# Optimization experiments

Measured on AMD Instinct MI355X. Metric: run time of the kernel, lower is better.

The kernel has to match this reference:

```python
import jax, jax.numpy as jnp
import numpy as np

N = 100000
E = 1600000
IN_DIM = 256
OUT_DIM = 128
LEAKY_SLOPE = 0.01  # torch nn.LeakyReLU default


def setup_inputs() -> dict:
    key = jax.random.key(0)
    k1, k2, k3, k4, k5 = jax.random.split(key, 5)
    features = jax.random.normal(k1, (N, IN_DIM), dtype=jnp.float32)
    # xavier_uniform for weight [out, in]
    limit = float(np.sqrt(6.0 / (IN_DIM + OUT_DIM)))
    weight = jax.random.uniform(k2, (OUT_DIM, IN_DIM), dtype=jnp.float32,
                                minval=-limit, maxval=limit)
    edge_rows = jnp.sort(jax.random.randint(k3, (E,), 0, N, dtype=jnp.int32))
    edge_cols = jax.random.randint(k4, (E,), 0, N, dtype=jnp.int32)
    edge_vals = jax.random.uniform(k5, (E,), dtype=jnp.float32)
    return {"features": features, "weight": weight,
            "edge_rows": edge_rows, "edge_cols": edge_cols,
            "edge_vals": edge_vals}


def reference(features, weight, edge_rows, edge_cols, edge_vals):
    # support = LeakyReLU(features @ W^T)   [N, OUT_DIM]
    support = jax.nn.leaky_relu(jnp.einsum('ni,oi->no', features, weight),
                                negative_slope=LEAKY_SLOPE)
    # SpMM: out[r] = sum over edges (r, c, v) of v * support[c]
    msgs = support[edge_cols] * edge_vals[:, None]  # [E, OUT_DIM]
    out = jax.ops.segment_sum(msgs, edge_rows, num_segments=N)
    return out
```

## Files before the change

### kernel.cpp

```cpp
#include <hip/hip_runtime.h>

#define IN_DIM 256
#define OUT_DIM 128
#define LEAKY 0.01f
#define GEMM_BLOCKS 512

typedef __attribute__((ext_vector_type(8))) short bf16x8;
typedef __attribute__((ext_vector_type(4))) float f32x4;
typedef __attribute__((ext_vector_type(4))) unsigned u32x4;

__device__ inline unsigned cvtpk_bf16(float lo, float hi) {
  unsigned r;
  asm volatile("v_cvt_pk_bf16_f32 %0, %1, %2" : "=v"(r) : "v"(lo), "v"(hi));
  return r;
}

__device__ inline float blo(unsigned u) {
  union { unsigned x; float f; } c; c.x = u << 16; return c.f;
}
__device__ inline float bhi(unsigned u) {
  union { unsigned x; float f; } c; c.x = u & 0xFFFF0000u; return c.f;
}
__device__ inline float asf(unsigned u) {
  union { unsigned x; float f; } c; c.x = u; return c.f;
}

__device__ inline int swz_byte(int r, int u) {
  return r * 512 + ((u & 16) << 4) + (((u & 15) ^ (r & 15)) << 4);
}

__global__ __launch_bounds__(512, 4) void gemm_scan_pack(
    const float* __restrict__ feat, const float* __restrict__ w,
    const int* __restrict__ erows, const int* __restrict__ ecols,
    const float* __restrict__ evals, unsigned short* __restrict__ support,
    int* __restrict__ rs, unsigned* __restrict__ ev, int nrows, int nedges,
    int ntiles, int scan_blocks) {
  if (blockIdx.x >= GEMM_BLOCKS) {
    const int sb = blockIdx.x - GEMM_BLOCKS;
    if (sb < scan_blocks) {
      const int i = sb * 512 + threadIdx.x;
      if (i >= nedges) return;
      const int cur  = erows[i];
      const int prev = (i == 0) ? -1 : erows[i - 1];
      for (int r = prev + 1; r <= cur; ++r) rs[r] = i;
      if (i == nedges - 1)
        for (int r = cur + 1; r <= nrows; ++r) rs[r] = nedges;
    } else {
      const int p = (sb - scan_blocks) * 512 + threadIdx.x;
      if (p * 2 + 1 >= nedges) {
        if (p * 2 < nedges) {
          ev[p * 4 + 0] = (unsigned)ecols[p * 2];
          ev[p * 4 + 1] = __float_as_uint(evals[p * 2]);
        }
        return;
      }
      const int2   c2 = *reinterpret_cast<const int2*>(&ecols[p * 2]);
      const float2 v2 = *reinterpret_cast<const float2*>(&evals[p * 2]);
      uint4 o;
      o.x = (unsigned)c2.x;
      o.y = __float_as_uint(v2.x);
      o.z = (unsigned)c2.y;
      o.w = __float_as_uint(v2.y);
      reinterpret_cast<uint4*>(ev)[p] = o;
    }
    return;
  }

  __shared__ alignas(16) unsigned short wlds[128 * 256];
  char* wb = reinterpret_cast<char*>(wlds);

  const int t = threadIdx.x;
#pragma unroll
  for (int it = 0; it < 8; ++it) {
    const int g = it * 512 + t;
    const int r = g >> 5;
    const int u = g & 31;
    const float* src = w + r * IN_DIM + u * 8;
    const float4 a = *reinterpret_cast<const float4*>(src);
    const float4 b = *reinterpret_cast<const float4*>(src + 4);
    uint4 pk;
    pk.x = cvtpk_bf16(a.x, a.y);
    pk.y = cvtpk_bf16(a.z, a.w);
    pk.z = cvtpk_bf16(b.x, b.y);
    pk.w = cvtpk_bf16(b.z, b.w);
    *reinterpret_cast<uint4*>(wb + swz_byte(r, u)) = pk;
  }
  __syncthreads();

  const int wid  = t >> 6;
  const int lane = t & 63;
  const int lrow = lane & 15;
  const int hi   = lane >> 4;

  for (int tile = blockIdx.x; tile < ntiles; tile += GEMM_BLOCKS) {
    const int mrow = tile * 128 + wid * 16 + lrow;
    const int mr   = mrow < nrows ? mrow : nrows - 1;
    const float* fp = feat + mr * IN_DIM + hi * 8;

    f32x4 acc[8];
#pragma unroll
    for (int nt = 0; nt < 8; ++nt) acc[nt] = (f32x4){0.f, 0.f, 0.f, 0.f};

#pragma unroll
    for (int ks = 0; ks < 8; ++ks) {
      const float4 a = *reinterpret_cast<const float4*>(fp + ks * 32);
      const float4 b = *reinterpret_cast<const float4*>(fp + ks * 32 + 4);
      union { bf16x8 v; unsigned u[4]; } bf;
      bf.u[0] = cvtpk_bf16(a.x, a.y);
      bf.u[1] = cvtpk_bf16(a.z, a.w);
      bf.u[2] = cvtpk_bf16(b.x, b.y);
      bf.u[3] = cvtpk_bf16(b.z, b.w);
      const int u = ks * 4 + hi;
#pragma unroll
      for (int nt = 0; nt < 8; ++nt) {
        const bf16x8 af = *reinterpret_cast<const bf16x8*>(
            wb + swz_byte(nt * 16 + lrow, u));
        acc[nt] = __builtin_amdgcn_mfma_f32_16x16x32_bf16(af, bf.v, acc[nt],
                                                          0, 0, 0);
      }
    }

    if (mrow < nrows) {
      unsigned short* orow = support + mrow * OUT_DIM + hi * 4;
#pragma unroll
      for (int nt = 0; nt < 8; ++nt) {
        f32x4 v = acc[nt];
        float a0 = v[0] > 0.f ? v[0] : LEAKY * v[0];
        float a1 = v[1] > 0.f ? v[1] : LEAKY * v[1];
        float a2 = v[2] > 0.f ? v[2] : LEAKY * v[2];
        float a3 = v[3] > 0.f ? v[3] : LEAKY * v[3];
        uint2 st;
        st.x = cvtpk_bf16(a0, a1);
        st.y = cvtpk_bf16(a2, a3);
        *reinterpret_cast<uint2*>(orow + nt * 16) = st;
      }
    }
  }
}

__global__ __launch_bounds__(256) void spmm_bf16(
    const int* __restrict__ rs, const unsigned* __restrict__ ev,
    const unsigned short* __restrict__ support, float* __restrict__ out,
    int nrows, int nedges) {
  const int t    = threadIdx.x;
  const int lane = t & 15;
  const int row  = blockIdx.x * 16 + (t >> 4);
  if (row >= nrows) return;

  const int s = rs[row];
  const int e = rs[row + 1];

  f32x4 accA[4], accB[4];
#pragma unroll
  for (int j = 0; j < 4; ++j) {
    accA[j] = (f32x4){0.f, 0.f, 0.f, 0.f};
    accB[j] = (f32x4){0.f, 0.f, 0.f, 0.f};
  }

  const unsigned short* srow = support + lane * 8;
  const uint4* ev4 = reinterpret_cast<const uint4*>(ev);
  const int maxp = (nedges >> 1) - 1;

  for (int i = s & ~1; i < e; i += 8) {
    uint4 P[4];
    int   pg[4];
#pragma unroll
    for (int g = 0; g < 4; ++g) {
      int p = (i >> 1) + g;
      pg[g] = p < maxp ? p : maxp;
      P[g]  = ev4[pg[g]];
    }
#pragma unroll
    for (int j = 0; j < 8; ++j) {
      const int g    = j >> 1;
      const int idx  = pg[g] * 2 + (j & 1);
      const bool ok  = idx >= s && idx < e && idx >= i + 2 * g;
      const unsigned cu = (j & 1) ? P[g].z : P[g].x;
      const unsigned vu = (j & 1) ? P[g].w : P[g].y;
      const float v  = ok ? asf(vu) : 0.f;
      const u32x4 u =
          *reinterpret_cast<const u32x4*>(srow + (size_t)cu * OUT_DIM);
      const int k = j & 3;
      accA[k][0] += v * blo(u[0]);
      accA[k][1] += v * bhi(u[0]);
      accA[k][2] += v * blo(u[1]);
      accA[k][3] += v * bhi(u[1]);
      accB[k][0] += v * blo(u[2]);
      accB[k][1] += v * bhi(u[2]);
      accB[k][2] += v * blo(u[3]);
      accB[k][3] += v * bhi(u[3]);
    }
  }

#pragma unroll
  for (int j = 1; j < 4; ++j) {
    accA[0] += accA[j];
    accB[0] += accB[j];
  }
  float* orow = out + (size_t)row * OUT_DIM + lane * 8;
  __builtin_nontemporal_store(accA[0], reinterpret_cast<f32x4*>(orow));
  __builtin_nontemporal_store(accB[0], reinterpret_cast<f32x4*>(orow + 4));
}

extern "C" void kernel_launch(void* const* d_in, const int* in_sizes, int n_in,
                              void* d_out, int out_size, void* d_ws,
                              size_t ws_size, hipStream_t stream) {
  const float* features = (const float*)d_in[0];
  const float* weight   = (const float*)d_in[1];
  const int*   erows    = (const int*)d_in[2];
  const int*   ecols    = (const int*)d_in[3];
  const float* evals    = (const float*)d_in[4];
  float*       out      = (float*)d_out;

  const int nrows  = in_sizes[0] / IN_DIM;
  const int nedges = in_sizes[2];

  const size_t sup_bytes = (size_t)nrows * OUT_DIM * 2;
  const size_t rs_bytes  = (((size_t)(nrows + 1) * 4 + 15) / 16) * 16;
  unsigned short* support = (unsigned short*)d_ws;
  int*      rs = (int*)((char*)d_ws + sup_bytes);
  unsigned* ev = (unsigned*)((char*)d_ws + sup_bytes + rs_bytes);

  const int ntiles      = (nrows + 127) / 128;
  const int scan_blocks = (nedges + 511) / 512;
  const int pack_blocks = ((nedges / 2) + 511) / 512;

  gemm_scan_pack<<<GEMM_BLOCKS + scan_blocks + pack_blocks, 512, 0, stream>>>(
      features, weight, erows, ecols, evals, support, rs, ev, nrows, nedges,
      ntiles, scan_blocks);
  spmm_bf16<<<(nrows + 15) / 16, 256, 0, stream>>>(rs, ev, support, out,
                                                   nrows, nedges);
}
```

Baseline: 101.9 us.

## Slice support into column panels and split SpMM across slices

```diff
diff --git a/kernel.cpp b/kernel.cpp
--- a/kernel.cpp
+++ b/kernel.cpp
@@ -4,6 +4,7 @@
 #define OUT_DIM 128
 #define LEAKY 0.01f
 #define GEMM_BLOCKS 512
+#define NSLICE 8
 
 typedef __attribute__((ext_vector_type(8))) short bf16x8;
 typedef __attribute__((ext_vector_type(4))) float f32x4;
@@ -91,6 +92,7 @@
   const int lane = t & 63;
   const int lrow = lane & 15;
   const int hi   = lane >> 4;
+  const size_t slice_stride = (size_t)nrows * 16;
 
   for (int tile = blockIdx.x; tile < ntiles; tile += GEMM_BLOCKS) {
     const int mrow = tile * 128 + wid * 16 + lrow;
@@ -121,7 +123,6 @@
     }
 
     if (mrow < nrows) {
-      unsigned short* orow = support + mrow * OUT_DIM + hi * 4;
 #pragma unroll
       for (int nt = 0; nt < 8; ++nt) {
         f32x4 v = acc[nt];
@@ -132,74 +133,64 @@
         uint2 st;
         st.x = cvtpk_bf16(a0, a1);
         st.y = cvtpk_bf16(a2, a3);
-        *reinterpret_cast<uint2*>(orow + nt * 16) = st;
+        unsigned short* o =
+            support + nt * slice_stride + (size_t)mrow * 16 + hi * 4;
+        *reinterpret_cast<uint2*>(o) = st;
       }
     }
   }
 }
 
-__global__ __launch_bounds__(256) void spmm_bf16(
-    const int* __restrict__ rs, const unsigned* __restrict__ ev,
+__global__ __launch_bounds__(256) void spmm_sliced(
+    const int* __restrict__ rs, const uint2* __restrict__ ev,
     const unsigned short* __restrict__ support, float* __restrict__ out,
-    int nrows, int nedges) {
-  const int t    = threadIdx.x;
-  const int lane = t & 15;
-  const int row  = blockIdx.x * 16 + (t >> 4);
+    int nrows) {
+  const int t     = threadIdx.x;
+  const int s     = blockIdx.x & (NSLICE - 1);
+  const int chunk = blockIdx.x >> 3;
+  const int row   = chunk * 16 + (t >> 4);
+  const int lq    = t & 15;
+  const int j     = lq >> 1;
+  const int h     = lq & 1;
   if (row >= nrows) return;
 
-  const int s = rs[row];
-  const int e = rs[row + 1];
-
-  f32x4 accA[4], accB[4];
-#pragma unroll
-  for (int j = 0; j < 4; ++j) {
-    accA[j] = (f32x4){0.f, 0.f, 0.f, 0.f};
-    accB[j] = (f32x4){0.f, 0.f, 0.f, 0.f};
-  }
-
-  const unsigned short* srow = support + lane * 8;
-  const uint4* ev4 = reinterpret_cast<const uint4*>(ev);
-  const int maxp = (nedges >> 1) - 1;
-
-  for (int i = s & ~1; i < e; i += 8) {
-    uint4 P[4];
-    int   pg[4];
-#pragma unroll
-    for (int g = 0; g < 4; ++g) {
-      int p = (i >> 1) + g;
-      pg[g] = p < maxp ? p : maxp;
-      P[g]  = ev4[pg[g]];
-    }
-#pragma unroll
-    for (int j = 0; j < 8; ++j) {
-      const int g    = j >> 1;
-      const int idx  = pg[g] * 2 + (j & 1);
-      const bool ok  = idx >= s && idx < e && idx >= i + 2 * g;
-      const unsigned cu = (j & 1) ? P[g].z : P[g].x;
-      const unsigned vu = (j & 1) ? P[g].w : P[g].y;
-      const float v  = ok ? asf(vu) : 0.f;
-      const u32x4 u =
-          *reinterpret_cast<const u32x4*>(srow + (size_t)cu * OUT_DIM);
-      const int k = j & 3;
-      accA[k][0] += v * blo(u[0]);
-      accA[k][1] += v * bhi(u[0]);
-      accA[k][2] += v * blo(u[1]);
-      accA[k][3] += v * bhi(u[1]);
-      accB[k][0] += v * blo(u[2]);
-      accB[k][1] += v * bhi(u[2]);
-      accB[k][2] += v * blo(u[3]);
-      accB[k][3] += v * bhi(u[3]);
-    }
-  }
-
-#pragma unroll
-  for (int j = 1; j < 4; ++j) {
-    accA[0] += accA[j];
-    accB[0] += accB[j];
-  }
-  float* orow = out + (size_t)row * OUT_DIM + lane * 8;
-  __builtin_nontemporal_store(accA[0], reinterpret_cast<f32x4*>(orow));
-  __builtin_nontemporal_store(accB[0], reinterpret_cast<f32x4*>(orow + 4));
+  const int es = rs[row];
+  const int ee = rs[row + 1];
+  const unsigned short* sbase = support + (size_t)s * nrows * 16 + h * 8;
+
+  f32x4 a0 = {0.f, 0.f, 0.f, 0.f}, a1 = {0.f, 0.f, 0.f, 0.f};
+
+  for (int base = es; base < ee; base += 8) {
+    const int  idx = base + j;
+    const bool ok  = idx < ee;
+    const uint2 p  = ev[ok ? idx : ee - 1];
+    const float v  = ok ? asf(p.y) : 0.f;
+    const u32x4 u =
+        *reinterpret_cast<const u32x4*>(sbase + (size_t)p.x * 16);
+    a0[0] += v * blo(u[0]);
+    a0[1] += v * bhi(u[0]);
+    a0[2] += v * blo(u[1]);
+    a0[3] += v * bhi(u[1]);
+    a1[0] += v * blo(u[2]);
+    a1[1] += v * bhi(u[2]);
+    a1[2] += v * blo(u[3]);
+    a1[3] += v * bhi(u[3]);
+  }
+
+#pragma unroll
+  for (int m = 2; m <= 8; m <<= 1) {
+#pragma unroll
+    for (int k = 0; k < 4; ++k) {
+      a0[k] += __shfl_xor(a0[k], m);
+      a1[k] += __shfl_xor(a1[k], m);
+    }
+  }
+
+  if (j == 0) {
+    float* o = out + (size_t)row * OUT_DIM + s * 16 + h * 8;
+    __builtin_nontemporal_store(a0, reinterpret_cast<f32x4*>(o));
+    __builtin_nontemporal_store(a1, reinterpret_cast<f32x4*>(o + 4));
+  }
 }
 
 extern "C" void kernel_launch(void* const* d_in, const int* in_sizes, int n_in,
@@ -228,6 +219,8 @@
   gemm_scan_pack<<<GEMM_BLOCKS + scan_blocks + pack_blocks, 512, 0, stream>>>(
       features, weight, erows, ecols, evals, support, rs, ev, nrows, nedges,
       ntiles, scan_blocks);
-  spmm_bf16<<<(nrows + 15) / 16, 256, 0, stream>>>(rs, ev, support, out,
-                                                   nrows, nedges);
-}
+
+  const int chunks = (nrows + 15) / 16;
+  spmm_sliced<<<chunks * NSLICE, 256, 0, stream>>>(
+      rs, reinterpret_cast<const uint2*>(ev), support, out, nrows);
+}
```

New measurement: 127.2 us. +24.9%, slower.
